# Kernel tuning notes

Measured on AMD Instinct MI355X. Metric: run time of the kernel, lower is better.

## Reference

```python
import jax, jax.numpy as jnp
import numpy as np
import math

D = 768      # dim_model
H = 12       # num_heads
DK = D // H  # dim_q = dim_k = 64
F = 3072     # dim_feedforward
B, S = 4, 2048
EPS = 1e-5


def layer_norm(x, gamma, beta):
    mu = jnp.mean(x, axis=-1, keepdims=True)
    var = jnp.mean(jnp.square(x - mu), axis=-1, keepdims=True)
    return (x - mu) * jax.lax.rsqrt(var + EPS) * gamma + beta


def setup_inputs() -> dict:
    key = jax.random.key(0)
    ks = jax.random.split(key, 16)
    s = 0.02
    return {
        "source": jax.random.normal(ks[0], (B, S, D), jnp.float32),
        # per-head QKV projections stacked over heads: [H, D, DK]
        "Wq": jax.random.normal(ks[1], (H, D, DK), jnp.float32) * s,
        "bq": jnp.zeros((H, DK), jnp.float32),
        "Wk": jax.random.normal(ks[2], (H, D, DK), jnp.float32) * s,
        "bk": jnp.zeros((H, DK), jnp.float32),
        "Wv": jax.random.normal(ks[3], (H, D, DK), jnp.float32) * s,
        "bv": jnp.zeros((H, DK), jnp.float32),
        "Wo": jax.random.normal(ks[4], (H * DK, D), jnp.float32) * s,
        "bo": jnp.zeros((D,), jnp.float32),
        "g1": jnp.ones((D,), jnp.float32),
        "be1": jnp.zeros((D,), jnp.float32),
        "W1": jax.random.normal(ks[5], (D, F), jnp.float32) * s,
        "bf1": jnp.zeros((F,), jnp.float32),
        "W2": jax.random.normal(ks[6], (F, D), jnp.float32) * s,
        "bf2": jnp.zeros((D,), jnp.float32),
        "g2": jnp.ones((D,), jnp.float32),
        "be2": jnp.zeros((D,), jnp.float32),
    }


def reference(source, Wq, bq, Wk, bk, Wv, bv, Wo, bo, g1, be1, W1, bf1, W2, bf2, g2, be2):
    x = source
    # batched-over-heads QKV (original loops over heads; same math)
    q = jnp.einsum("bsd,hdk->bhsk", x, Wq) + bq[:, None, :]
    k = jnp.einsum("bsd,hdk->bhsk", x, Wk) + bk[:, None, :]
    v = jnp.einsum("bsd,hdk->bhsk", x, Wv) + bv[:, None, :]
    scale = math.sqrt(DK)
    scores = jnp.einsum("bhsk,bhtk->bhst", q, k) / scale  # [B,H,S,S]
    probs = jax.nn.softmax(scores, axis=-1)
    attn = jnp.einsum("bhst,bhtk->bhsk", probs, v)        # [B,H,S,DK]
    # concat heads along feature dim: [B,S,H*DK]
    cat = attn.transpose(0, 2, 1, 3).reshape(B, S, H * DK)
    mha = cat @ Wo + bo
    x1 = layer_norm(x + mha, g1, be1)  # dropout=0 / eval mode
    ffn = jax.nn.relu(x1 @ W1 + bf1) @ W2 + bf2
    return layer_norm(x1 + ffn, g2, be2)
```

## Files before the change

kernel.cpp:

```cpp
#include <hip/hip_runtime.h>
#include <stdint.h>

#define B_ 4
#define S_ 2048
#define D_ 768
#define H_ 12
#define DK_ 64
#define F_ 3072

typedef __bf16 bf16x8 __attribute__((ext_vector_type(8)));
typedef unsigned short u16x8 __attribute__((ext_vector_type(8)));
typedef float f32x4 __attribute__((ext_vector_type(4)));

__device__ inline unsigned short f2bf(float f) {
    union { float f; unsigned u; } v; v.f = f;
    unsigned r = (v.u + 0x7FFFu + ((v.u >> 16) & 1u)) >> 16;
    return (unsigned short)r;
}
__device__ inline float b2f(unsigned short u) {
    union { unsigned u; float f; } v; v.u = ((unsigned)u) << 16;
    return v.f;
}
__device__ inline bf16x8 as_bf(u16x8 v) { return __builtin_bit_cast(bf16x8, v); }
__device__ inline f32x4 mfma16(u16x8 a, u16x8 b, f32x4 c) {
    return __builtin_amdgcn_mfma_f32_16x16x32_bf16(as_bf(a), as_bf(b), c, 0, 0, 0);
}
__device__ inline void gld16(const unsigned short* g, unsigned short* l) {
    __builtin_amdgcn_global_load_lds(
        (__attribute__((address_space(1))) void*)(unsigned short*)g,
        (__attribute__((address_space(3))) void*)l, 16, 0, 0);
}
__device__ inline float fast_exp2(float x) { return __builtin_amdgcn_exp2f(x); }

__global__ __launch_bounds__(256) void cvt_k(const float* __restrict__ in,
                                             unsigned short* __restrict__ out, int n) {
    int i = (blockIdx.x * 256 + threadIdx.x) * 4;
    if (i >= n) return;
    float4 v = *(const float4*)(in + i);
    out[i] = f2bf(v.x); out[i+1] = f2bf(v.y); out[i+2] = f2bf(v.z); out[i+3] = f2bf(v.w);
}

__global__ __launch_bounds__(256) void bias_k(const float* __restrict__ bq,
                                              const float* __restrict__ bk,
                                              const float* __restrict__ bv,
                                              float* __restrict__ out) {
    int i = blockIdx.x * 256 + threadIdx.x;
    if (i >= 2304) return;
    const float* s = (i < 768) ? bq : (i < 1536 ? bk : bv);
    out[i] = s[i % 768];
}

__global__ __launch_bounds__(256) void tconv_k(const float* __restrict__ in,
                                               unsigned short* __restrict__ out,
                                               int inRS, int outRS, long inBS, long outBS) {
    __shared__ float tile[32][33];
    const float* ip = in + (long)blockIdx.z * inBS;
    unsigned short* op = out + (long)blockIdx.z * outBS;
    const int c0 = blockIdx.x * 32, r0 = blockIdx.y * 32;
    const int tx = threadIdx.x, ty = threadIdx.y;
    #pragma unroll
    for (int i = 0; i < 32; i += 8)
        tile[ty + i][tx] = ip[(long)(r0 + ty + i) * inRS + c0 + tx];
    __syncthreads();
    #pragma unroll
    for (int i = 0; i < 32; i += 8)
        op[(long)(c0 + ty + i) * outRS + r0 + tx] = f2bf(tile[tx][ty + i]);
}

template<bool OUTBF, bool RELU, bool HASRES>
__global__ __launch_bounds__(256, 2) void gemm_k(const unsigned short* __restrict__ A,
                                                 const unsigned short* __restrict__ Bt,
                                                 const float* __restrict__ bias,
                                                 const float* __restrict__ res,
                                                 void* __restrict__ outp,
                                                 int M, int N, int K) {
    __shared__ unsigned short As[4096];
    __shared__ unsigned short Bs[4096];
    const int tid = threadIdx.x;
    const int w = tid >> 6, lane = tid & 63;
    const int m = lane & 15, quad = lane >> 4;
    const int wm = (w >> 1) * 64, wn = (w & 1) * 64;
    const long m0 = (long)blockIdx.x * 128, n0 = (long)blockIdx.y * 128;

    const int rowc = tid >> 2, colc = (tid & 3) * 8;
    const unsigned short* aG0 = A + (m0 + rowc) * K + colc;
    const unsigned short* aG1 = A + (m0 + rowc + 64) * K + colc;
    const unsigned short* bG0 = Bt + (n0 + rowc) * K + colc;
    const unsigned short* bG1 = Bt + (n0 + rowc + 64) * K + colc;
    unsigned short* lA0 = As + w * 512;
    unsigned short* lA1 = As + 2048 + w * 512;
    unsigned short* lB0 = Bs + w * 512;
    unsigned short* lB1 = Bs + 2048 + w * 512;

    const f32x4 fz = {0.f, 0.f, 0.f, 0.f};
    f32x4 acc[4][4];
    #pragma unroll
    for (int i = 0; i < 4; i++)
        #pragma unroll
        for (int j = 0; j < 4; j++) acc[i][j] = fz;

    for (int k0 = 0; k0 < K; k0 += 32) {
        __syncthreads();
        gld16(aG0 + k0, lA0);
        gld16(aG1 + k0, lA1);
        gld16(bG0 + k0, lB0);
        gld16(bG1 + k0, lB1);
        __syncthreads();
        u16x8 af[4], bfr[4];
        #pragma unroll
        for (int i = 0; i < 4; i++) af[i] = *(const u16x8*)&As[(wm + i*16 + m)*32 + quad*8];
        #pragma unroll
        for (int j = 0; j < 4; j++) bfr[j] = *(const u16x8*)&Bs[(wn + j*16 + m)*32 + quad*8];
        #pragma unroll
        for (int i = 0; i < 4; i++)
            #pragma unroll
            for (int j = 0; j < 4; j++)
                acc[i][j] = mfma16(af[i], bfr[j], acc[i][j]);
    }

    #pragma unroll
    for (int j = 0; j < 4; j++) {
        const long col = n0 + wn + j*16 + m;
        const float bv = bias[col];
        #pragma unroll
        for (int i = 0; i < 4; i++) {
            #pragma unroll
            for (int r = 0; r < 4; r++) {
                const long row = m0 + wm + i*16 + quad*4 + r;
                float v = acc[i][j][r] + bv;
                if (HASRES) v += res[row * N + col];
                if (RELU)   v = fmaxf(v, 0.0f);
                if (OUTBF)  ((unsigned short*)outp)[row * N + col] = f2bf(v);
                else        ((float*)outp)[row * N + col] = v;
            }
        }
    }
}

template<bool OUTBF, bool RELU, bool HASRES>
__global__ __launch_bounds__(256, 4) void gemm2_k(const unsigned short* __restrict__ A,
                                                  const unsigned short* __restrict__ Bt,
                                                  const float* __restrict__ bias,
                                                  const float* __restrict__ res,
                                                  void* __restrict__ outp,
                                                  int M, int N, int K) {
    __shared__ unsigned short As[4096];
    __shared__ unsigned short Bs[2048];
    const int tid = threadIdx.x;
    const int w = tid >> 6, lane = tid & 63;
    const int m = lane & 15, quad = lane >> 4;
    const int wm = (w >> 1) * 64, wn = (w & 1) * 32;
    const long m0 = (long)blockIdx.x * 128, n0 = (long)blockIdx.y * 64;

    const int rowc = tid >> 2, colc = (tid & 3) * 8;
    const unsigned short* aG0 = A + (m0 + rowc) * K + colc;
    const unsigned short* aG1 = A + (m0 + rowc + 64) * K + colc;
    const unsigned short* bG0 = Bt + (n0 + rowc) * K + colc;
    unsigned short* lA0 = As + w * 512;
    unsigned short* lA1 = As + 2048 + w * 512;
    unsigned short* lB0 = Bs + w * 512;

    const f32x4 fz = {0.f, 0.f, 0.f, 0.f};
    f32x4 acc[4][2];
    #pragma unroll
    for (int i = 0; i < 4; i++)
        #pragma unroll
        for (int j = 0; j < 2; j++) acc[i][j] = fz;

    for (int k0 = 0; k0 < K; k0 += 32) {
        __syncthreads();
        gld16(aG0 + k0, lA0);
        gld16(aG1 + k0, lA1);
        gld16(bG0 + k0, lB0);
        __syncthreads();
        u16x8 af[4], bfr[2];
        #pragma unroll
        for (int i = 0; i < 4; i++) af[i] = *(const u16x8*)&As[(wm + i*16 + m)*32 + quad*8];
        #pragma unroll
        for (int j = 0; j < 2; j++) bfr[j] = *(const u16x8*)&Bs[(wn + j*16 + m)*32 + quad*8];
        #pragma unroll
        for (int i = 0; i < 4; i++)
            #pragma unroll
            for (int j = 0; j < 2; j++)
                acc[i][j] = mfma16(af[i], bfr[j], acc[i][j]);
    }

    #pragma unroll
    for (int j = 0; j < 2; j++) {
        const long col = n0 + wn + j*16 + m;
        const float bv = bias[col];
        #pragma unroll
        for (int i = 0; i < 4; i++) {
            #pragma unroll
            for (int r = 0; r < 4; r++) {
                const long row = m0 + wm + i*16 + quad*4 + r;
                float v = acc[i][j][r] + bv;
                if (HASRES) v += res[row * N + col];
                if (RELU)   v = fmaxf(v, 0.0f);
                if (OUTBF)  ((unsigned short*)outp)[row * N + col] = f2bf(v);
                else        ((float*)outp)[row * N + col] = v;
            }
        }
    }
}

__global__ __launch_bounds__(256, 3) void attn_k(const unsigned short* __restrict__ qkv,
                                                 unsigned short* __restrict__ cat) {
    __shared__ unsigned short Kl[2][4096];
    __shared__ unsigned short Vt[2][64 * 68];
    __shared__ unsigned short Pl[4][32 * 72];

    const int tid = threadIdx.x, w = tid >> 6, lane = tid & 63;
    const int m = lane & 15, quad = lane >> 4;
    const int b = blockIdx.y / H_, h = blockIdx.y % H_;
    const int q0 = blockIdx.x * 128 + w * 32;
    const long rb = (long)b * S_;
    const int LD = 3 * D_;

    const unsigned short* kb = qkv + rb * (long)LD + h * DK_ + D_;
    const unsigned short* vb = qkv + rb * (long)LD + h * DK_ + 2 * D_;

    const int krow = tid >> 2, kcol = (tid & 3) * 8;

    const float QS = 0.125f * 1.4426950408889634f;
    u16x8 qf[2][2];
    #pragma unroll
    for (int s = 0; s < 2; s++)
        #pragma unroll
        for (int ks = 0; ks < 2; ks++) {
            const unsigned short* qp = qkv + (rb + q0 + s*16 + m) * (long)LD + h*DK_ + ks*32 + quad*8;
            u16x8 raw = *(const u16x8*)qp;
            u16x8 sc;
            #pragma unroll
            for (int j = 0; j < 8; j++) sc[j] = f2bf(b2f(raw[j]) * QS);
            qf[s][ks] = sc;
        }

    const int vpr = (tid >> 3) * 2;
    const int vd  = (tid & 7) * 8;

    gld16(kb + (long)krow * LD + kcol,      &Kl[0][w * 512]);
    gld16(kb + (long)krow * LD + 32 + kcol, &Kl[0][2048 + w * 512]);
    {
        u16x8 v0 = *(const u16x8*)(vb + (long)(vpr)     * LD + vd);
        u16x8 v1 = *(const u16x8*)(vb + (long)(vpr + 1) * LD + vd);
        #pragma unroll
        for (int j = 0; j < 8; j++) {
            unsigned pk = (unsigned)v0[j] | ((unsigned)v1[j] << 16);
            *(unsigned*)&Vt[0][(vd + j)*68 + vpr] = pk;
        }
    }

    const f32x4 fz = {0.f, 0.f, 0.f, 0.f};
    float lrow[2] = {0.f, 0.f};
    f32x4 oacc[2][4];
    #pragma unroll
    for (int s = 0; s < 2; s++)
        #pragma unroll
        for (int o = 0; o < 4; o++) oacc[s][o] = fz;

    const int NC = S_ / 64;
    for (int c = 0; c < NC; c++) {
        const int kv0 = c * 64;
        const bool havenext = (c + 1 < NC);
        __syncthreads();

        const unsigned short* kcur = Kl[c & 1];
        const unsigned short* vcur = Vt[c & 1];

        if (havenext) {
            unsigned short* kn_ = Kl[(c + 1) & 1];
            gld16(kb + (long)(kv0 + 64 + krow) * LD + kcol,      kn_ + w * 512);
            gld16(kb + (long)(kv0 + 64 + krow) * LD + 32 + kcol, kn_ + 2048 + w * 512);
        }
        const int kvn = havenext ? kv0 + 64 : kv0;
        u16x8 nv0 = *(const u16x8*)(vb + (long)(kvn + vpr)     * LD + vd);
        u16x8 nv1 = *(const u16x8*)(vb + (long)(kvn + vpr + 1) * LD + vd);

        f32x4 st[2][4];
        #pragma unroll
        for (int s = 0; s < 2; s++)
            #pragma unroll
            for (int t = 0; t < 4; t++) st[s][t] = fz;
        #pragma unroll
        for (int t = 0; t < 4; t++) {
            u16x8 kf0 = *(const u16x8*)&kcur[(t*16 + m)*32 + quad*8];
            u16x8 kf1 = *(const u16x8*)&kcur[2048 + (t*16 + m)*32 + quad*8];
            st[0][t] = mfma16(kf0, qf[0][0], st[0][t]);
            st[0][t] = mfma16(kf1, qf[0][1], st[0][t]);
            st[1][t] = mfma16(kf0, qf[1][0], st[1][t]);
            st[1][t] = mfma16(kf1, qf[1][1], st[1][t]);
        }

        #pragma unroll
        for (int s = 0; s < 2; s++) {
            float su = 0.f;
            #pragma unroll
            for (int t = 0; t < 4; t++) {
                float p0 = fast_exp2(st[s][t][0]);
                float p1 = fast_exp2(st[s][t][1]);
                float p2 = fast_exp2(st[s][t][2]);
                float p3 = fast_exp2(st[s][t][3]);
                su += (p0 + p1) + (p2 + p3);
                unsigned a0 = __builtin_bit_cast(unsigned, p0) + 0x8000u;
                unsigned a1 = __builtin_bit_cast(unsigned, p1) + 0x8000u;
                unsigned a2 = __builtin_bit_cast(unsigned, p2) + 0x8000u;
                unsigned a3 = __builtin_bit_cast(unsigned, p3) + 0x8000u;
                uint2 pk;
                pk.x = __builtin_amdgcn_perm(a1, a0, 0x07060302u);
                pk.y = __builtin_amdgcn_perm(a3, a2, 0x07060302u);
                *(uint2*)&Pl[w][(s*16 + m)*72 + t*16 + quad*4] = pk;
            }
            lrow[s] += su;
        }

        __asm__ volatile("s_waitcnt lgkmcnt(0)" ::: "memory");

        u16x8 pf[2][2];
        #pragma unroll
        for (int s = 0; s < 2; s++)
            #pragma unroll
            for (int ks = 0; ks < 2; ks++)
                pf[s][ks] = *(const u16x8*)&Pl[w][(s*16 + m)*72 + ks*32 + quad*8];

        #pragma unroll
        for (int o = 0; o < 4; o++)
            #pragma unroll
            for (int ks = 0; ks < 2; ks++) {
                union { u16x8 v; uint2 d[2]; } vf;
                vf.d[0] = *(const uint2*)&vcur[(o*16 + m)*68 + ks*32 + quad*8];
                vf.d[1] = *(const uint2*)&vcur[(o*16 + m)*68 + ks*32 + quad*8 + 4];
                oacc[0][o] = mfma16(pf[0][ks], vf.v, oacc[0][o]);
                oacc[1][o] = mfma16(pf[1][ks], vf.v, oacc[1][o]);
            }

        if (havenext) {
            unsigned short* vtn = Vt[(c + 1) & 1];
            #pragma unroll
            for (int j = 0; j < 8; j++) {
                unsigned pk = (unsigned)nv0[j] | ((unsigned)nv1[j] << 16);
                *(unsigned*)&vtn[(vd + j)*68 + vpr] = pk;
            }
        }
    }

    #pragma unroll
    for (int s = 0; s < 2; s++) {
        lrow[s] += __shfl_xor(lrow[s], 16);
        lrow[s] += __shfl_xor(lrow[s], 32);
    }
    #pragma unroll
    for (int s = 0; s < 2; s++) {
        float inv[4];
        #pragma unroll
        for (int r = 0; r < 4; r++) inv[r] = 1.0f / __shfl(lrow[s], quad*4 + r);
        #pragma unroll
        for (int o = 0; o < 4; o++)
            #pragma unroll
            for (int r = 0; r < 4; r++) {
                float v = oacc[s][o][r] * inv[r];
                cat[(rb + q0 + s*16 + quad*4 + r) * (long)D_ + h*DK_ + o*16 + m] = f2bf(v);
            }
    }
}

__global__ __launch_bounds__(256) void ln_k(const float* __restrict__ in,
                                            const float* __restrict__ g,
                                            const float* __restrict__ be,
                                            float* __restrict__ outF,
                                            unsigned short* __restrict__ outB) {
    __shared__ float sm[4], sm2[4];
    const int t = threadIdx.x, w = t >> 6, lane = t & 63;
    const long row = blockIdx.x;
    const float* x = in + row * D_;
    float v0 = x[t], v1 = x[t + 256], v2 = x[t + 512];
    float s = v0 + v1 + v2;
    float s2 = v0*v0 + v1*v1 + v2*v2;
    #pragma unroll
    for (int off = 32; off >= 1; off >>= 1) {
        s  += __shfl_xor(s,  off, 64);
        s2 += __shfl_xor(s2, off, 64);
    }
    if (lane == 0) { sm[w] = s; sm2[w] = s2; }
    __syncthreads();
    s  = sm[0] + sm[1] + sm[2] + sm[3];
    s2 = sm2[0] + sm2[1] + sm2[2] + sm2[3];
    const float mu = s * (1.0f / D_);
    float var = s2 * (1.0f / D_) - mu * mu;
    var = fmaxf(var, 0.0f);
    const float rs = rsqrtf(var + 1e-5f);
    #pragma unroll
    for (int i = 0; i < 3; i++) {
        const int idx = t + i * 256;
        const float vv = (i == 0 ? v0 : (i == 1 ? v1 : v2));
        const float y = (vv - mu) * rs * g[idx] + be[idx];
        if (outF) outF[row * D_ + idx] = y;
        if (outB) outB[row * D_ + idx] = f2bf(y);
    }
}

extern "C" void kernel_launch(void* const* d_in, const int* in_sizes, int n_in,
                              void* d_out, int out_size, void* d_ws, size_t ws_size,
                              hipStream_t stream) {
    const float* src = (const float*)d_in[0];
    const float* Wq  = (const float*)d_in[1];
    const float* bq  = (const float*)d_in[2];
    const float* Wk  = (const float*)d_in[3];
    const float* bk  = (const float*)d_in[4];
    const float* Wv  = (const float*)d_in[5];
    const float* bv  = (const float*)d_in[6];
    const float* Wo  = (const float*)d_in[7];
    const float* bo  = (const float*)d_in[8];
    const float* g1  = (const float*)d_in[9];
    const float* be1 = (const float*)d_in[10];
    const float* W1  = (const float*)d_in[11];
    const float* bf1 = (const float*)d_in[12];
    const float* W2  = (const float*)d_in[13];
    const float* bf2 = (const float*)d_in[14];
    const float* g2  = (const float*)d_in[15];
    const float* be2 = (const float*)d_in[16];
    float* out = (float*)d_out;

    char* ws = (char*)d_ws;
    unsigned short* XBF  = (unsigned short*)(ws);
    unsigned short* CAT  = (unsigned short*)(ws + 12582912);
    unsigned short* QKV  = (unsigned short*)(ws + 25165824);
    float*          Y1   = (float*)(ws + 25165824);
    unsigned short* WQT  = (unsigned short*)(ws + 62914560);
    unsigned short* WOT  = (unsigned short*)(ws + 66453504);
    unsigned short* W1T  = (unsigned short*)(ws + 67633152);
    unsigned short* W2T  = (unsigned short*)(ws + 72351744);
    float*          BQKV = (float*)(ws + 77070336);
    float*          X1R  = (float*)(ws + 77079552);
    unsigned short* X1B  = (unsigned short*)(ws + 102245376);
    unsigned short* Hb   = (unsigned short*)(ws + 114828288);

    cvt_k<<<dim3(6144), 256, 0, stream>>>(src, XBF, 6291456);
    bias_k<<<dim3(9), 256, 0, stream>>>(bq, bk, bv, BQKV);
    dim3 tb(32, 8);
    tconv_k<<<dim3(2, 24, 12), tb, 0, stream>>>(Wq, WQT,                64, 768, 49152L, 49152L);
    tconv_k<<<dim3(2, 24, 12), tb, 0, stream>>>(Wk, WQT + 589824,       64, 768, 49152L, 49152L);
    tconv_k<<<dim3(2, 24, 12), tb, 0, stream>>>(Wv, WQT + 1179648,      64, 768, 49152L, 49152L);
    tconv_k<<<dim3(24, 24, 1), tb, 0, stream>>>(Wo, WOT,                768, 768, 0L, 0L);
    tconv_k<<<dim3(96, 24, 1), tb, 0, stream>>>(W1, W1T,                3072, 768, 0L, 0L);
    tconv_k<<<dim3(24, 96, 1), tb, 0, stream>>>(W2, W2T,                768, 3072, 0L, 0L);

    gemm_k<true, false, false><<<dim3(64, 18), 256, 0, stream>>>(XBF, WQT, BQKV, nullptr, QKV, 8192, 2304, 768);
    attn_k<<<dim3(16, 48), 256, 0, stream>>>(QKV, CAT);
    gemm2_k<false, false, true><<<dim3(64, 12), 256, 0, stream>>>(CAT, WOT, bo, src, Y1, 8192, 768, 768);
    ln_k<<<dim3(8192), 256, 0, stream>>>(Y1, g1, be1, X1R, X1B);
    gemm_k<true, true, false><<<dim3(64, 24), 256, 0, stream>>>(X1B, W1T, bf1, nullptr, Hb, 8192, 3072, 768);
    gemm2_k<false, false, true><<<dim3(64, 12), 256, 0, stream>>>(Hb, W2T, bf2, X1R, out, 8192, 768, 3072);
    ln_k<<<dim3(8192), 256, 0, stream>>>(out, g2, be2, out, nullptr);
}
```

Baseline: 435.5 us.

## Merge prep kernels, deepen GEMM k-step, split-K FFN2 with LN reduction

```diff
diff --git a/kernel.cpp b/kernel.cpp
--- a/kernel.cpp
+++ b/kernel.cpp
@@ -32,32 +32,71 @@
 }
 __device__ inline float fast_exp2(float x) { return __builtin_amdgcn_exp2f(x); }
 
-__global__ __launch_bounds__(256) void cvt_k(const float* __restrict__ in,
-                                             unsigned short* __restrict__ out, int n) {
-    int i = (blockIdx.x * 256 + threadIdx.x) * 4;
-    if (i >= n) return;
-    float4 v = *(const float4*)(in + i);
-    out[i] = f2bf(v.x); out[i+1] = f2bf(v.y); out[i+2] = f2bf(v.z); out[i+3] = f2bf(v.w);
-}
-
-__global__ __launch_bounds__(256) void bias_k(const float* __restrict__ bq,
+__global__ __launch_bounds__(256) void prep_k(const float* __restrict__ src,
+                                              unsigned short* __restrict__ XBF,
+                                              const float* __restrict__ bq,
                                               const float* __restrict__ bk,
                                               const float* __restrict__ bv,
-                                              float* __restrict__ out) {
-    int i = blockIdx.x * 256 + threadIdx.x;
-    if (i >= 2304) return;
-    const float* s = (i < 768) ? bq : (i < 1536 ? bk : bv);
-    out[i] = s[i % 768];
-}
-
-__global__ __launch_bounds__(256) void tconv_k(const float* __restrict__ in,
-                                               unsigned short* __restrict__ out,
-                                               int inRS, int outRS, long inBS, long outBS) {
+                                              float* __restrict__ BQKV,
+                                              const float* __restrict__ Wq,
+                                              const float* __restrict__ Wk,
+                                              const float* __restrict__ Wv,
+                                              const float* __restrict__ Wo,
+                                              const float* __restrict__ W1,
+                                              const float* __restrict__ W2,
+                                              unsigned short* __restrict__ WQT,
+                                              unsigned short* __restrict__ WOT,
+                                              unsigned short* __restrict__ W1T,
+                                              unsigned short* __restrict__ W2T) {
     __shared__ float tile[32][33];
-    const float* ip = in + (long)blockIdx.z * inBS;
-    unsigned short* op = out + (long)blockIdx.z * outBS;
-    const int c0 = blockIdx.x * 32, r0 = blockIdx.y * 32;
-    const int tx = threadIdx.x, ty = threadIdx.y;
+    int bid = blockIdx.x;
+    const int t = threadIdx.x;
+
+    if (bid < 6144) {
+        int i = (bid * 256 + t) * 4;
+        float4 v = *(const float4*)(src + i);
+        XBF[i] = f2bf(v.x); XBF[i+1] = f2bf(v.y); XBF[i+2] = f2bf(v.z); XBF[i+3] = f2bf(v.w);
+        return;
+    }
+    bid -= 6144;
+    if (bid < 9) {
+        int i = bid * 256 + t;
+        if (i < 2304) {
+            const float* s = (i < 768) ? bq : (i < 1536 ? bk : bv);
+            BQKV[i] = s[i % 768];
+        }
+        return;
+    }
+    bid -= 9;
+
+    const float* ip; unsigned short* op;
+    int inRS, outRS, bx, by;
+    if (bid < 1728) {
+        int sel = bid / 576; int rem = bid - sel * 576;
+        int z = rem / 48; int r2 = rem - z * 48;
+        by = r2 >> 1; bx = r2 & 1;
+        ip  = (sel == 0 ? Wq : (sel == 1 ? Wk : Wv)) + (long)z * 49152;
+        op  = WQT + (long)sel * 589824 + (long)z * 49152;
+        inRS = 64; outRS = 768;
+    } else {
+        bid -= 1728;
+        if (bid < 576) {
+            by = bid / 24; bx = bid - by * 24;
+            ip = Wo; op = WOT; inRS = 768; outRS = 768;
+        } else {
+            bid -= 576;
+            if (bid < 2304) {
+                by = bid / 96; bx = bid - by * 96;
+                ip = W1; op = W1T; inRS = 3072; outRS = 768;
+            } else {
+                bid -= 2304;
+                by = bid / 24; bx = bid - by * 24;
+                ip = W2; op = W2T; inRS = 768; outRS = 3072;
+            }
+        }
+    }
+    const int c0 = bx * 32, r0 = by * 32;
+    const int tx = t & 31, ty = t >> 5;
     #pragma unroll
     for (int i = 0; i < 32; i += 8)
         tile[ty + i][tx] = ip[(long)(r0 + ty + i) * inRS + c0 + tx];
@@ -67,30 +106,34 @@
         op[(long)(c0 + ty + i) * outRS + r0 + tx] = f2bf(tile[tx][ty + i]);
 }
 
-template<bool OUTBF, bool RELU, bool HASRES>
+template<bool OUTBF, bool RELU, bool HASRES, bool SPLIT2>
 __global__ __launch_bounds__(256, 2) void gemm_k(const unsigned short* __restrict__ A,
                                                  const unsigned short* __restrict__ Bt,
                                                  const float* __restrict__ bias,
                                                  const float* __restrict__ res,
                                                  void* __restrict__ outp,
+                                                 float* __restrict__ outp2,
                                                  int M, int N, int K) {
-    __shared__ unsigned short As[4096];
-    __shared__ unsigned short Bs[4096];
+    __shared__ unsigned short As[8192];
+    __shared__ unsigned short Bs[8192];
     const int tid = threadIdx.x;
     const int w = tid >> 6, lane = tid & 63;
     const int m = lane & 15, quad = lane >> 4;
     const int wm = (w >> 1) * 64, wn = (w & 1) * 64;
     const long m0 = (long)blockIdx.x * 128, n0 = (long)blockIdx.y * 128;
 
+    int koff = 0, kend = K;
+    bool lead = true;
+    if (SPLIT2) {
+        const int Kh = K >> 1, z = blockIdx.z;
+        koff = z * Kh; kend = koff + Kh; lead = (z == 0);
+    }
+
     const int rowc = tid >> 2, colc = (tid & 3) * 8;
     const unsigned short* aG0 = A + (m0 + rowc) * K + colc;
     const unsigned short* aG1 = A + (m0 + rowc + 64) * K + colc;
     const unsigned short* bG0 = Bt + (n0 + rowc) * K + colc;
     const unsigned short* bG1 = Bt + (n0 + rowc + 64) * K + colc;
-    unsigned short* lA0 = As + w * 512;
-    unsigned short* lA1 = As + 2048 + w * 512;
-    unsigned short* lB0 = Bs + w * 512;
-    unsigned short* lB1 = Bs + 2048 + w * 512;
 
     const f32x4 fz = {0.f, 0.f, 0.f, 0.f};
     f32x4 acc[4][4];
@@ -99,106 +142,52 @@
         #pragma unroll
         for (int j = 0; j < 4; j++) acc[i][j] = fz;
 
-    for (int k0 = 0; k0 < K; k0 += 32) {
+    for (int k0 = koff; k0 < kend; k0 += 64) {
         __syncthreads();
-        gld16(aG0 + k0, lA0);
-        gld16(aG1 + k0, lA1);
-        gld16(bG0 + k0, lB0);
-        gld16(bG1 + k0, lB1);
+        #pragma unroll
+        for (int ks = 0; ks < 2; ks++) {
+            const int kc = k0 + ks * 32;
+            gld16(aG0 + kc, As + ks*4096 + w*512);
+            gld16(aG1 + kc, As + ks*4096 + 2048 + w*512);
+            gld16(bG0 + kc, Bs + ks*4096 + w*512);
+            gld16(bG1 + kc, Bs + ks*4096 + 2048 + w*512);
+        }
         __syncthreads();
-        u16x8 af[4], bfr[4];
-        #pragma unroll
-        for (int i = 0; i < 4; i++) af[i] = *(const u16x8*)&As[(wm + i*16 + m)*32 + quad*8];
-        #pragma unroll
-        for (int j = 0; j < 4; j++) bfr[j] = *(const u16x8*)&Bs[(wn + j*16 + m)*32 + quad*8];
-        #pragma unroll
-        for (int i = 0; i < 4; i++)
-            #pragma unroll
-            for (int j = 0; j < 4; j++)
-                acc[i][j] = mfma16(af[i], bfr[j], acc[i][j]);
+        #pragma unroll
+        for (int ks = 0; ks < 2; ks++) {
+            u16x8 af[4], bfr[4];
+            #pragma unroll
+            for (int i = 0; i < 4; i++) af[i] = *(const u16x8*)&As[ks*4096 + (wm + i*16 + m)*32 + quad*8];
+            #pragma unroll
+            for (int j = 0; j < 4; j++) bfr[j] = *(const u16x8*)&Bs[ks*4096 + (wn + j*16 + m)*32 + quad*8];
+            #pragma unroll
+            for (int i = 0; i < 4; i++)
+                #pragma unroll
+                for (int j = 0; j < 4; j++)
+                    acc[i][j] = mfma16(af[i], bfr[j], acc[i][j]);
+        }
     }
 
     #pragma unroll
     for (int j = 0; j < 4; j++) {
         const long col = n0 + wn + j*16 + m;
-        const float bv = bias[col];
+        const float bv = lead ? bias[col] : 0.0f;
         #pragma unroll
         for (int i = 0; i < 4; i++) {
             #pragma unroll
             for (int r = 0; r < 4; r++) {
                 const long row = m0 + wm + i*16 + quad*4 + r;
                 float v = acc[i][j][r] + bv;
-                if (HASRES) v += res[row * N + col];
+                if (HASRES) { if (lead) v += res[row * N + col]; }
                 if (RELU)   v = fmaxf(v, 0.0f);
-                if (OUTBF)  ((unsigned short*)outp)[row * N + col] = f2bf(v);
-                else        ((float*)outp)[row * N + col] = v;
-            }
-        }
-    }
-}
-
-template<bool OUTBF, bool RELU, bool HASRES>
-__global__ __launch_bounds__(256, 4) void gemm2_k(const unsigned short* __restrict__ A,
-                                                  const unsigned short* __restrict__ Bt,
-                                                  const float* __restrict__ bias,
-                                                  const float* __restrict__ res,
-                                                  void* __restrict__ outp,
-                                                  int M, int N, int K) {
-    __shared__ unsigned short As[4096];
-    __shared__ unsigned short Bs[2048];
-    const int tid = threadIdx.x;
-    const int w = tid >> 6, lane = tid & 63;
-    const int m = lane & 15, quad = lane >> 4;
-    const int wm = (w >> 1) * 64, wn = (w & 1) * 32;
-    const long m0 = (long)blockIdx.x * 128, n0 = (long)blockIdx.y * 64;
-
-    const int rowc = tid >> 2, colc = (tid & 3) * 8;
-    const unsigned short* aG0 = A + (m0 + rowc) * K + colc;
-    const unsigned short* aG1 = A + (m0 + rowc + 64) * K + colc;
-    const unsigned short* bG0 = Bt + (n0 + rowc) * K + colc;
-    unsigned short* lA0 = As + w * 512;
-    unsigned short* lA1 = As + 2048 + w * 512;
-    unsigned short* lB0 = Bs + w * 512;
-
-    const f32x4 fz = {0.f, 0.f, 0.f, 0.f};
-    f32x4 acc[4][2];
-    #pragma unroll
-    for (int i = 0; i < 4; i++)
-        #pragma unroll
-        for (int j = 0; j < 2; j++) acc[i][j] = fz;
-
-    for (int k0 = 0; k0 < K; k0 += 32) {
-        __syncthreads();
-        gld16(aG0 + k0, lA0);
-        gld16(aG1 + k0, lA1);
-        gld16(bG0 + k0, lB0);
-        __syncthreads();
-        u16x8 af[4], bfr[2];
-        #pragma unroll
-        for (int i = 0; i < 4; i++) af[i] = *(const u16x8*)&As[(wm + i*16 + m)*32 + quad*8];
-        #pragma unroll
-        for (int j = 0; j < 2; j++) bfr[j] = *(const u16x8*)&Bs[(wn + j*16 + m)*32 + quad*8];
-        #pragma unroll
-        for (int i = 0; i < 4; i++)
-            #pragma unroll
-            for (int j = 0; j < 2; j++)
-                acc[i][j] = mfma16(af[i], bfr[j], acc[i][j]);
-    }
-
-    #pragma unroll
-    for (int j = 0; j < 2; j++) {
-        const long col = n0 + wn + j*16 + m;
-        const float bv = bias[col];
-        #pragma unroll
-        for (int i = 0; i < 4; i++) {
-            #pragma unroll
-            for (int r = 0; r < 4; r++) {
-                const long row = m0 + wm + i*16 + quad*4 + r;
-                float v = acc[i][j][r] + bv;
-                if (HASRES) v += res[row * N + col];
-                if (RELU)   v = fmaxf(v, 0.0f);
-                if (OUTBF)  ((unsigned short*)outp)[row * N + col] = f2bf(v);
-                else        ((float*)outp)[row * N + col] = v;
+                if (SPLIT2) {
+                    float* o = lead ? (float*)outp : outp2;
+                    o[row * N + col] = v;
+                } else if (OUTBF) {
+                    ((unsigned short*)outp)[row * N + col] = f2bf(v);
+                } else {
+                    ((float*)outp)[row * N + col] = v;
+                }
             }
         }
     }
@@ -365,6 +354,7 @@
 }
 
 __global__ __launch_bounds__(256) void ln_k(const float* __restrict__ in,
+                                            const float* __restrict__ in2,
                                             const float* __restrict__ g,
                                             const float* __restrict__ be,
                                             float* __restrict__ outF,
@@ -374,6 +364,10 @@
     const long row = blockIdx.x;
     const float* x = in + row * D_;
     float v0 = x[t], v1 = x[t + 256], v2 = x[t + 512];
+    if (in2) {
+        const float* y = in2 + row * D_;
+        v0 += y[t]; v1 += y[t + 256]; v2 += y[t + 512];
+    }
     float s = v0 + v1 + v2;
     float s2 = v0*v0 + v1*v1 + v2*v2;
     #pragma unroll
@@ -423,6 +417,7 @@
 
     char* ws = (char*)d_ws;
     unsigned short* XBF  = (unsigned short*)(ws);
+    float*          P1F2 = (float*)(ws);
     unsigned short* CAT  = (unsigned short*)(ws + 12582912);
     unsigned short* QKV  = (unsigned short*)(ws + 25165824);
     float*          Y1   = (float*)(ws + 25165824);
@@ -435,21 +430,19 @@
     unsigned short* X1B  = (unsigned short*)(ws + 102245376);
     unsigned short* Hb   = (unsigned short*)(ws + 114828288);
 
-    cvt_k<<<dim3(6144), 256, 0, stream>>>(src, XBF, 6291456);
-    bias_k<<<dim3(9), 256, 0, stream>>>(bq, bk, bv, BQKV);
-    dim3 tb(32, 8);
-    tconv_k<<<dim3(2, 24, 12), tb, 0, stream>>>(Wq, WQT,                64, 768, 49152L, 49152L);
-    tconv_k<<<dim3(2, 24, 12), tb, 0, stream>>>(Wk, WQT + 589824,       64, 768, 49152L, 49152L);
-    tconv_k<<<dim3(2, 24, 12), tb, 0, stream>>>(Wv, WQT + 1179648,      64, 768, 49152L, 49152L);
-    tconv_k<<<dim3(24, 24, 1), tb, 0, stream>>>(Wo, WOT,                768, 768, 0L, 0L);
-    tconv_k<<<dim3(96, 24, 1), tb, 0, stream>>>(W1, W1T,                3072, 768, 0L, 0L);
-    tconv_k<<<dim3(24, 96, 1), tb, 0, stream>>>(W2, W2T,                768, 3072, 0L, 0L);
-
-    gemm_k<true, false, false><<<dim3(64, 18), 256, 0, stream>>>(XBF, WQT, BQKV, nullptr, QKV, 8192, 2304, 768);
+    prep_k<<<dim3(13065), 256, 0, stream>>>(src, XBF, bq, bk, bv, BQKV,
+                                            Wq, Wk, Wv, Wo, W1, W2,
+                                            WQT, WOT, W1T, W2T);
+
+    gemm_k<true, false, false, false><<<dim3(64, 18), 256, 0, stream>>>(
+        XBF, WQT, BQKV, nullptr, QKV, nullptr, 8192, 2304, 768);
     attn_k<<<dim3(16, 48), 256, 0, stream>>>(QKV, CAT);
-    gemm2_k<false, false, true><<<dim3(64, 12), 256, 0, stream>>>(CAT, WOT, bo, src, Y1, 8192, 768, 768);
-    ln_k<<<dim3(8192), 256, 0, stream>>>(Y1, g1, be1, X1R, X1B);
-    gemm_k<true, true, false><<<dim3(64, 24), 256, 0, stream>>>(X1B, W1T, bf1, nullptr, Hb, 8192, 3072, 768);
-    gemm2_k<false, false, true><<<dim3(64, 12), 256, 0, stream>>>(Hb, W2T, bf2, X1R, out, 8192, 768, 3072);
-    ln_k<<<dim3(8192), 256, 0, stream>>>(out, g2, be2, out, nullptr);
-}
+    gemm_k<false, false, true, false><<<dim3(64, 6), 256, 0, stream>>>(
+        CAT, WOT, bo, src, Y1, nullptr, 8192, 768, 768);
+    ln_k<<<dim3(8192), 256, 0, stream>>>(Y1, nullptr, g1, be1, X1R, X1B);
+    gemm_k<true, true, false, false><<<dim3(64, 24), 256, 0, stream>>>(
+        X1B, W1T, bf1, nullptr, Hb, nullptr, 8192, 3072, 768);
+    gemm_k<false, false, true, true><<<dim3(64, 6, 2), 256, 0, stream>>>(
+        Hb, W2T, bf2, X1R, Y1, P1F2, 8192, 768, 3072);
+    ln_k<<<dim3(8192), 256, 0, stream>>>(Y1, P1F2, g2, be2, out, nullptr);
+}
```

Result: faster. 394.6 us (-9.4%).
